# Optimization experiments

Measured on AMD Instinct MI355X. Metric: run time of the kernel, lower is better.

The kernel has to match this reference:

```python
import jax, jax.numpy as jnp
import numpy as np

B, N, S = 8, 512, 96
SD = TD = H = 256
NH, HD = 8, 32  # num_heads, head_dim
OUT = 4


def setup_inputs() -> dict:
    key = jax.random.key(0)
    ks = jax.random.split(key, 20)
    g = lambda k, shape: (jax.random.normal(k, shape, dtype=jnp.float32) * 0.02)
    return {
        "spatial_features": jax.random.normal(ks[0], (B, N, SD), dtype=jnp.float32),
        "temporal_features": jax.random.normal(ks[1], (B, S, TD), dtype=jnp.float32),
        "Ws": g(ks[2], (H, SD)),   "bs": g(ks[3], (H,)),
        "Wt": g(ks[4], (H, TD)),   "bt": g(ks[5], (H,)),
        "Win": g(ks[6], (3 * H, H)), "bin": g(ks[7], (3 * H,)),
        "Wao": g(ks[8], (H, H)),   "bao": g(ks[9], (H,)),
        "W1": g(ks[10], (H, H)),   "b1": g(ks[11], (H,)),
        "Wo1": g(ks[12], (H // 2, H)), "bo1": g(ks[13], (H // 2,)),
        "Wo2": g(ks[14], (OUT, H // 2)), "bo2": g(ks[15], (OUT,)),
    }


def reference(spatial_features, temporal_features, Ws, bs, Wt, bt, Win, bin, Wao, bao,
              W1, b1, Wo1, bo1, Wo2, bo2):
    # Projections
    sp = spatial_features @ Ws.T + bs          # [B, N, H]
    tp = temporal_features @ Wt.T + bt         # [B, S, H]
    # MultiheadAttention in_proj (batched over all N node-queries at once;
    # mathematically identical to the original per-node loop)
    Wq, Wk, Wv = Win[:H], Win[H:2 * H], Win[2 * H:]
    bq, bk, bv = bin[:H], bin[H:2 * H], bin[2 * H:]
    q = (sp @ Wq.T + bq).reshape(B, N, NH, HD)   # [B, N, h, d]
    k = (tp @ Wk.T + bk).reshape(B, S, NH, HD)   # [B, S, h, d]
    v = (tp @ Wv.T + bv).reshape(B, S, NH, HD)
    scale = 1.0 / np.sqrt(HD).astype(np.float32)
    logits = jnp.einsum('bnhd,bshd->bhns', q * scale, k)   # [B, h, N, S]
    attn = jax.nn.softmax(logits, axis=-1)
    ctx = jnp.einsum('bhns,bshd->bnhd', attn, v).reshape(B, N, H)
    attended = ctx @ Wao.T + bao               # [B, N, H] (out_proj)
    # fusion_layer: Linear + ReLU (dropout=identity in eval)
    fused = jax.nn.relu(attended @ W1.T + b1)  # [B, N, H]
    # output_layer: Linear -> ReLU -> Linear
    h2 = jax.nn.relu(fused @ Wo1.T + bo1)      # [B, N, H/2]
    y = h2 @ Wo2.T + bo2                       # [B, N, OUT]
    # original expands over seq_len BEFORE fusion_layer; since all layers are
    # pointwise over the (S, N) grid, compute once per node and broadcast.
    return jnp.broadcast_to(y[:, None, :, :], (B, S, N, OUT))
```

## Files before the change

kernel.cpp:

```cpp
#include <hip/hip_runtime.h>

#define BB 8
#define NN 512
#define SS 96
#define HH 256
#define NHD 8
#define HDD 32
#define OUTD 4

#define WSB_OFF  0
#define WTB_OFF  65536
#define WINB_OFF 131072
#define WAOB_OFF 327680
#define W1B_OFF  393216
#define WO1B_OFF 458752
#define BF_TOTAL 491520
#define QB_OFF   491520
#define KB_OFF   (QB_OFF + 1048576)
#define VTB_OFF  (KB_OFF + 196608)

typedef __attribute__((ext_vector_type(8))) short bf16x8;
typedef __attribute__((ext_vector_type(4))) float f32x4;

__device__ __forceinline__ unsigned short f2bf(float f) {
    unsigned int u = __float_as_uint(f);
    u = (u + 0x7FFFu + ((u >> 16) & 1u)) >> 16;
    return (unsigned short)u;
}

__global__ __launch_bounds__(256) void k_cast(
    const float* __restrict__ Ws, const float* __restrict__ Wt,
    const float* __restrict__ Win, const float* __restrict__ Wao,
    const float* __restrict__ W1, const float* __restrict__ Wo1,
    unsigned short* __restrict__ dst)
{
    int idx = blockIdx.x * 256 + threadIdx.x;
    for (int j4 = idx; j4 < BF_TOTAL / 4; j4 += 120 * 256) {
        int e = j4 * 4;
        const float* src; int off;
        if (e < 65536)       { src = Ws;  off = e; }
        else if (e < 131072) { src = Wt;  off = e - 65536; }
        else if (e < 327680) { src = Win; off = e - 131072; }
        else if (e < 393216) { src = Wao; off = e - 327680; }
        else if (e < 458752) { src = W1;  off = e - 393216; }
        else                 { src = Wo1; off = e - 458752; }
        float4 v = *(const float4*)(src + off);
        ushort4 o;
        o.x = f2bf(v.x); o.y = f2bf(v.y); o.z = f2bf(v.z); o.w = f2bf(v.w);
        *(ushort4*)(dst + e) = o;
    }
}

template<int NCT>
__device__ __forceinline__ void mfma_stage(
    const unsigned short* __restrict__ Asw,
    const unsigned short* __restrict__ Wb,
    int lane, int wave, f32x4 acc[NCT])
{
    const int row = lane & 15, kq = lane >> 4;
    #pragma unroll
    for (int ct = 0; ct < NCT; ++ct) acc[ct] = (f32x4){0.f, 0.f, 0.f, 0.f};
    #pragma unroll 2
    for (int kt = 0; kt < 8; ++kt) {
        const int slot = kt * 4 + kq;
        bf16x8 a = *(const bf16x8*)(Asw + row * 256 + ((slot ^ (row & 7)) << 3));
        #pragma unroll
        for (int ct = 0; ct < NCT; ++ct) {
            const unsigned short* wp =
                Wb + (size_t)((wave * NCT + ct) * 16 + row) * 256 + kt * 32 + kq * 8;
            bf16x8 b = *(const bf16x8*)wp;
            acc[ct] = __builtin_amdgcn_mfma_f32_16x16x32_bf16(a, b, acc[ct], 0, 0, 0);
        }
    }
}

template<int NCT, bool RELU>
__device__ __forceinline__ void epi_lds(
    unsigned short* __restrict__ OutSw, const float* __restrict__ bias,
    int lane, int wave, const f32x4 acc[NCT])
{
    const int col0 = lane & 15, rq = lane >> 4;
    #pragma unroll
    for (int ct = 0; ct < NCT; ++ct) {
        const int C = wave * NCT * 16 + ct * 16 + col0;
        const float bb = bias[C];
        const int slot = C >> 3, within = C & 7;
        #pragma unroll
        for (int r = 0; r < 4; ++r) {
            const int R = rq * 4 + r;
            float v = acc[ct][r] + bb;
            if (RELU) v = fmaxf(v, 0.f);
            OutSw[R * 256 + ((slot ^ (R & 7)) << 3) + within] = f2bf(v);
        }
    }
}

template<int NCT>
__device__ __forceinline__ void epi_gbf16(
    unsigned short* __restrict__ Og, const float* __restrict__ bias,
    int lane, int wave, const f32x4 acc[NCT])
{
    const int col0 = lane & 15, rq = lane >> 4;
    #pragma unroll
    for (int ct = 0; ct < NCT; ++ct) {
        const int C = wave * NCT * 16 + ct * 16 + col0;
        const float bb = bias[C];
        #pragma unroll
        for (int r = 0; r < 4; ++r) {
            const int R = rq * 4 + r;
            Og[(size_t)R * 256 + C] = f2bf(acc[ct][r] + bb);
        }
    }
}

__device__ __forceinline__ void stage_A(
    const float* __restrict__ Ag, unsigned short* __restrict__ Asw, int tid)
{
    #pragma unroll
    for (int ii = 0; ii < 4; ++ii) {
        int i = tid + ii * 256;
        int row = i >> 6, c4 = i & 63;
        float4 v = ((const float4*)(Ag + (size_t)row * 256))[c4];
        int col = c4 * 4;
        int slot = col >> 3, half = (col >> 2) & 1;
        ushort4 o;
        o.x = f2bf(v.x); o.y = f2bf(v.y); o.z = f2bf(v.z); o.w = f2bf(v.w);
        *(ushort4*)(Asw + row * 256 + ((slot ^ (row & 7)) << 3) + half * 4) = o;
    }
}

__global__ __launch_bounds__(256) void k_qkv(
    const float* __restrict__ spatial, const float* __restrict__ temporal,
    const float* __restrict__ bs, const float* __restrict__ bt,
    const float* __restrict__ bin,
    const unsigned short* __restrict__ bfw,
    unsigned short* __restrict__ qb, unsigned short* __restrict__ kb,
    unsigned short* __restrict__ vtb)
{
    __shared__ __align__(16) unsigned short A0[16 * 256];
    __shared__ __align__(16) unsigned short MID[16 * 256];
    const int tid = threadIdx.x, lane = tid & 63, wave = tid >> 6;
    f32x4 acc[4];

    if (blockIdx.x < 256) {
        const int r0 = blockIdx.x * 16;
        stage_A(spatial + (size_t)r0 * 256, A0, tid);
        __syncthreads();
        mfma_stage<4>(A0, bfw + WSB_OFF, lane, wave, acc);
        epi_lds<4, false>(MID, bs, lane, wave, acc);
        __syncthreads();
        mfma_stage<4>(MID, bfw + WINB_OFF, lane, wave, acc);
        epi_gbf16<4>(qb + (size_t)r0 * 256, bin, lane, wave, acc);
    } else {
        const int r0 = (blockIdx.x - 256) * 16;
        stage_A(temporal + (size_t)r0 * 256, A0, tid);
        __syncthreads();
        mfma_stage<4>(A0, bfw + WTB_OFF, lane, wave, acc);
        epi_lds<4, false>(MID, bt, lane, wave, acc);
        __syncthreads();
        mfma_stage<4>(MID, bfw + WINB_OFF + 65536, lane, wave, acc);
        epi_gbf16<4>(kb + (size_t)r0 * 256, bin + 256, lane, wave, acc);
        mfma_stage<4>(MID, bfw + WINB_OFF + 131072, lane, wave, acc);
        {
            const int bb_ = r0 / 96, s0 = r0 % 96;
            const int col0 = lane & 15, rq = lane >> 4;
            #pragma unroll
            for (int ct = 0; ct < 4; ++ct) {
                const int C = wave * 64 + ct * 16 + col0;
                const float bv = bin[512 + C];
                #pragma unroll
                for (int r = 0; r < 4; ++r) {
                    const int R = rq * 4 + r;
                    vtb[((size_t)(bb_ * 256 + C)) * 96 + s0 + R] = f2bf(acc[ct][r] + bv);
                }
            }
        }
    }
}

__global__ __launch_bounds__(256) void k_attnhead(
    const unsigned short* __restrict__ qb, const unsigned short* __restrict__ kb,
    const unsigned short* __restrict__ vtb, const unsigned short* __restrict__ bfw,
    const float* __restrict__ bao, const float* __restrict__ b1,
    const float* __restrict__ bo1,
    const float* __restrict__ Wo2, const float* __restrict__ bo2,
    float* __restrict__ out)
{
    __shared__ __align__(16) unsigned short A0[16 * 256];
    __shared__ __align__(16) unsigned short MID[16 * 256];
    __shared__ __align__(16) float H2[16 * 128];
    __shared__ __align__(16) unsigned short P[4][16 * 104];
    __shared__ __align__(16) float y[16][OUTD];
    const int tid = threadIdx.x, lane = tid & 63, wave = tid >> 6;
    const int b = blockIdx.x >> 5;
    const int n0 = (blockIdx.x & 31) * 16;
    const int cl = lane & 15, kq = lane >> 4;
    const float scale = 0.17677669529663687f;

    unsigned short* Pw = &P[wave][0];
    #pragma unroll
    for (int hh = 0; hh < 2; ++hh) {
        const int h = wave * 2 + hh;
        bf16x8 aq = *(const bf16x8*)(qb + (size_t)(b * NN + n0 + cl) * 256 + h * 32 + kq * 8);
        f32x4 l[6];
        #pragma unroll
        for (int t = 0; t < 6; ++t) {
            bf16x8 bk = *(const bf16x8*)(kb + (size_t)(b * SS + t * 16 + cl) * 256 + h * 32 + kq * 8);
            l[t] = __builtin_amdgcn_mfma_f32_16x16x32_bf16(aq, bk, (f32x4){0.f,0.f,0.f,0.f}, 0, 0, 0);
        }
        float pr[6][4];
        float sum[4] = {0.f, 0.f, 0.f, 0.f};
        #pragma unroll
        for (int t = 0; t < 6; ++t)
            #pragma unroll
            for (int r = 0; r < 4; ++r) {
                float p = __expf(l[t][r] * scale);
                pr[t][r] = p; sum[r] += p;
            }
        #pragma unroll
        for (int r = 0; r < 4; ++r) {
            float s = sum[r];
            s += __shfl_xor(s, 1); s += __shfl_xor(s, 2);
            s += __shfl_xor(s, 4); s += __shfl_xor(s, 8);
            sum[r] = 1.0f / s;
        }
        #pragma unroll
        for (int t = 0; t < 6; ++t)
            #pragma unroll
            for (int r = 0; r < 4; ++r)
                Pw[(kq * 4 + r) * 104 + t * 16 + cl] = f2bf(pr[t][r] * sum[r]);
        f32x4 c0 = (f32x4){0.f,0.f,0.f,0.f}, c1 = (f32x4){0.f,0.f,0.f,0.f};
        #pragma unroll
        for (int ks = 0; ks < 3; ++ks) {
            bf16x8 pa = *(const bf16x8*)(Pw + cl * 104 + ks * 32 + kq * 8);
            bf16x8 v0 = *(const bf16x8*)(vtb + (size_t)(b * 256 + h * 32 + cl) * 96 + ks * 32 + kq * 8);
            bf16x8 v1 = *(const bf16x8*)(vtb + (size_t)(b * 256 + h * 32 + 16 + cl) * 96 + ks * 32 + kq * 8);
            c0 = __builtin_amdgcn_mfma_f32_16x16x32_bf16(pa, v0, c0, 0, 0, 0);
            c1 = __builtin_amdgcn_mfma_f32_16x16x32_bf16(pa, v1, c1, 0, 0, 0);
        }
        #pragma unroll
        for (int dt = 0; dt < 2; ++dt) {
            const f32x4 cc = dt ? c1 : c0;
            const int C = h * 32 + dt * 16 + cl;
            const int slot = C >> 3, within = C & 7;
            #pragma unroll
            for (int r = 0; r < 4; ++r) {
                const int R = kq * 4 + r;
                A0[R * 256 + ((slot ^ (R & 7)) << 3) + within] = f2bf(cc[r]);
            }
        }
    }
    __syncthreads();

    f32x4 acc[4];
    mfma_stage<4>(A0, bfw + WAOB_OFF, lane, wave, acc);
    epi_lds<4, false>(MID, bao, lane, wave, acc);
    __syncthreads();
    mfma_stage<4>(MID, bfw + W1B_OFF, lane, wave, acc);
    epi_lds<4, true>(A0, b1, lane, wave, acc);
    __syncthreads();
    {
        f32x4 a2[2];
        mfma_stage<2>(A0, bfw + WO1B_OFF, lane, wave, a2);
        const int rq = lane >> 4;
        #pragma unroll
        for (int ct = 0; ct < 2; ++ct) {
            const int C = wave * 32 + ct * 16 + cl;
            const float bb = bo1[C];
            #pragma unroll
            for (int r = 0; r < 4; ++r) {
                const int R = rq * 4 + r;
                H2[R * 128 + C] = fmaxf(a2[ct][r] + bb, 0.f);
            }
        }
    }
    __syncthreads();
    if (tid < 64) {
        int r = tid >> 2, o = tid & 3;
        float a = 0.f;
        const float4* w4 = (const float4*)(Wo2 + (size_t)o * 128);
        const float4* h4 = (const float4*)(H2 + r * 128);
        for (int kk = 0; kk < 32; ++kk) {
            float4 w = w4[kk], hv = h4[kk];
            a += hv.x * w.x + hv.y * w.y + hv.z * w.z + hv.w * w.w;
        }
        y[r][o] = a + bo2[o];
    }
    __syncthreads();
    const int nbase = n0;
    for (int i = tid; i < 16 * SS; i += 256) {
        int s = i >> 4;
        int r = i & 15;
        *(float4*)(out + ((size_t)(b * SS + s) * NN + (nbase + r)) * OUTD) = *(const float4*)y[r];
    }
}

extern "C" void kernel_launch(void* const* d_in, const int* in_sizes, int n_in,
                              void* d_out, int out_size, void* d_ws, size_t ws_size,
                              hipStream_t stream) {
    const float* spatial  = (const float*)d_in[0];
    const float* temporal = (const float*)d_in[1];
    const float* Ws  = (const float*)d_in[2];
    const float* bs  = (const float*)d_in[3];
    const float* Wt  = (const float*)d_in[4];
    const float* bt  = (const float*)d_in[5];
    const float* Win = (const float*)d_in[6];
    const float* bin = (const float*)d_in[7];
    const float* Wao = (const float*)d_in[8];
    const float* bao = (const float*)d_in[9];
    const float* W1  = (const float*)d_in[10];
    const float* b1  = (const float*)d_in[11];
    const float* Wo1 = (const float*)d_in[12];
    const float* bo1 = (const float*)d_in[13];
    const float* Wo2 = (const float*)d_in[14];
    const float* bo2 = (const float*)d_in[15];
    float* out = (float*)d_out;
    unsigned short* wsu = (unsigned short*)d_ws;

    unsigned short* bfw = wsu;
    unsigned short* qb  = wsu + QB_OFF;
    unsigned short* kb  = wsu + KB_OFF;
    unsigned short* vtb = wsu + VTB_OFF;

    hipLaunchKernelGGL(k_cast, dim3(120), dim3(256), 0, stream,
                       Ws, Wt, Win, Wao, W1, Wo1, bfw);
    hipLaunchKernelGGL(k_qkv, dim3(304), dim3(256), 0, stream,
                       spatial, temporal, bs, bt, bin, bfw, qb, kb, vtb);
    hipLaunchKernelGGL(k_attnhead, dim3(256), dim3(256), 0, stream,
                       qb, kb, vtb, bfw, bao, b1, bo1, Wo2, bo2, out);
}
```

Baseline: 127.1 us.

## Fuse Q projection into attention kernel and merge weight cast with K/V prep

Moves the spatial projection and Q in-projection into the attention/head kernel, so Q stays in shared memory instead of going through global memory. The K/V projection now reads fp32 weights directly and casts them on the fly. It runs concurrently with the weight cast of the remaining matrices inside one kernel, which cuts three launches down to two. In exchange, each attention block does extra GEMM work before attention, and the K/V blocks redundantly convert weights per load.

```diff
diff --git a/kernel.cpp b/kernel.cpp
--- a/kernel.cpp
+++ b/kernel.cpp
@@ -9,15 +9,13 @@
 #define OUTD 4
 
 #define WSB_OFF  0
-#define WTB_OFF  65536
-#define WINB_OFF 131072
-#define WAOB_OFF 327680
-#define W1B_OFF  393216
-#define WO1B_OFF 458752
-#define BF_TOTAL 491520
-#define QB_OFF   491520
-#define KB_OFF   (QB_OFF + 1048576)
-#define VTB_OFF  (KB_OFF + 196608)
+#define WQB_OFF  65536
+#define WAOB_OFF 131072
+#define W1B_OFF  196608
+#define WO1B_OFF 262144
+#define CAST_TOTAL 294912
+#define KB_OFF   294912
+#define VTB_OFF  491520
 
 typedef __attribute__((ext_vector_type(8))) short bf16x8;
 typedef __attribute__((ext_vector_type(4))) float f32x4;
@@ -28,27 +26,14 @@
     return (unsigned short)u;
 }
 
-__global__ __launch_bounds__(256) void k_cast(
-    const float* __restrict__ Ws, const float* __restrict__ Wt,
-    const float* __restrict__ Win, const float* __restrict__ Wao,
-    const float* __restrict__ W1, const float* __restrict__ Wo1,
-    unsigned short* __restrict__ dst)
-{
-    int idx = blockIdx.x * 256 + threadIdx.x;
-    for (int j4 = idx; j4 < BF_TOTAL / 4; j4 += 120 * 256) {
-        int e = j4 * 4;
-        const float* src; int off;
-        if (e < 65536)       { src = Ws;  off = e; }
-        else if (e < 131072) { src = Wt;  off = e - 65536; }
-        else if (e < 327680) { src = Win; off = e - 131072; }
-        else if (e < 393216) { src = Wao; off = e - 327680; }
-        else if (e < 458752) { src = W1;  off = e - 393216; }
-        else                 { src = Wo1; off = e - 458752; }
-        float4 v = *(const float4*)(src + off);
-        ushort4 o;
-        o.x = f2bf(v.x); o.y = f2bf(v.y); o.z = f2bf(v.z); o.w = f2bf(v.w);
-        *(ushort4*)(dst + e) = o;
-    }
+__device__ __forceinline__ bf16x8 ldw8(const float* __restrict__ p) {
+    float4 a = *(const float4*)p, b = *(const float4*)(p + 4);
+    bf16x8 r;
+    r[0] = (short)f2bf(a.x); r[1] = (short)f2bf(a.y);
+    r[2] = (short)f2bf(a.z); r[3] = (short)f2bf(a.w);
+    r[4] = (short)f2bf(b.x); r[5] = (short)f2bf(b.y);
+    r[6] = (short)f2bf(b.z); r[7] = (short)f2bf(b.w);
+    return r;
 }
 
 template<int NCT>
@@ -69,6 +54,29 @@
             const unsigned short* wp =
                 Wb + (size_t)((wave * NCT + ct) * 16 + row) * 256 + kt * 32 + kq * 8;
             bf16x8 b = *(const bf16x8*)wp;
+            acc[ct] = __builtin_amdgcn_mfma_f32_16x16x32_bf16(a, b, acc[ct], 0, 0, 0);
+        }
+    }
+}
+
+template<int NCT>
+__device__ __forceinline__ void mfma_stage_f32w(
+    const unsigned short* __restrict__ Asw,
+    const float* __restrict__ Wf,
+    int lane, int wave, f32x4 acc[NCT])
+{
+    const int row = lane & 15, kq = lane >> 4;
+    #pragma unroll
+    for (int ct = 0; ct < NCT; ++ct) acc[ct] = (f32x4){0.f, 0.f, 0.f, 0.f};
+    #pragma unroll 2
+    for (int kt = 0; kt < 8; ++kt) {
+        const int slot = kt * 4 + kq;
+        bf16x8 a = *(const bf16x8*)(Asw + row * 256 + ((slot ^ (row & 7)) << 3));
+        #pragma unroll
+        for (int ct = 0; ct < NCT; ++ct) {
+            const float* wp =
+                Wf + (size_t)((wave * NCT + ct) * 16 + row) * 256 + kt * 32 + kq * 8;
+            bf16x8 b = ldw8(wp);
             acc[ct] = __builtin_amdgcn_mfma_f32_16x16x32_bf16(a, b, acc[ct], 0, 0, 0);
         }
     }
@@ -129,38 +137,30 @@
     }
 }
 
-__global__ __launch_bounds__(256) void k_qkv(
-    const float* __restrict__ spatial, const float* __restrict__ temporal,
-    const float* __restrict__ bs, const float* __restrict__ bt,
-    const float* __restrict__ bin,
-    const unsigned short* __restrict__ bfw,
-    unsigned short* __restrict__ qb, unsigned short* __restrict__ kb,
-    unsigned short* __restrict__ vtb)
-{
-    __shared__ __align__(16) unsigned short A0[16 * 256];
-    __shared__ __align__(16) unsigned short MID[16 * 256];
-    const int tid = threadIdx.x, lane = tid & 63, wave = tid >> 6;
-    f32x4 acc[4];
-
-    if (blockIdx.x < 256) {
+__global__ __launch_bounds__(256) void k_prep(
+    const float* __restrict__ temporal,
+    const float* __restrict__ bt, const float* __restrict__ bin,
+    const float* __restrict__ Wt, const float* __restrict__ Win,
+    const float* __restrict__ Ws, const float* __restrict__ Wao,
+    const float* __restrict__ W1, const float* __restrict__ Wo1,
+    unsigned short* __restrict__ kb, unsigned short* __restrict__ vtb,
+    unsigned short* __restrict__ bfw)
+{
+    const int tid = threadIdx.x;
+    if (blockIdx.x < 48) {
+        __shared__ __align__(16) unsigned short A0[16 * 256];
+        __shared__ __align__(16) unsigned short MID[16 * 256];
+        const int lane = tid & 63, wave = tid >> 6;
         const int r0 = blockIdx.x * 16;
-        stage_A(spatial + (size_t)r0 * 256, A0, tid);
-        __syncthreads();
-        mfma_stage<4>(A0, bfw + WSB_OFF, lane, wave, acc);
-        epi_lds<4, false>(MID, bs, lane, wave, acc);
-        __syncthreads();
-        mfma_stage<4>(MID, bfw + WINB_OFF, lane, wave, acc);
-        epi_gbf16<4>(qb + (size_t)r0 * 256, bin, lane, wave, acc);
-    } else {
-        const int r0 = (blockIdx.x - 256) * 16;
+        f32x4 acc[4];
         stage_A(temporal + (size_t)r0 * 256, A0, tid);
         __syncthreads();
-        mfma_stage<4>(A0, bfw + WTB_OFF, lane, wave, acc);
+        mfma_stage_f32w<4>(A0, Wt, lane, wave, acc);
         epi_lds<4, false>(MID, bt, lane, wave, acc);
         __syncthreads();
-        mfma_stage<4>(MID, bfw + WINB_OFF + 65536, lane, wave, acc);
+        mfma_stage_f32w<4>(MID, Win + 65536, lane, wave, acc);
         epi_gbf16<4>(kb + (size_t)r0 * 256, bin + 256, lane, wave, acc);
-        mfma_stage<4>(MID, bfw + WINB_OFF + 131072, lane, wave, acc);
+        mfma_stage_f32w<4>(MID, Win + 131072, lane, wave, acc);
         {
             const int bb_ = r0 / 96, s0 = r0 % 96;
             const int col0 = lane & 15, rq = lane >> 4;
@@ -175,12 +175,29 @@
                 }
             }
         }
-    }
-}
-
-__global__ __launch_bounds__(256) void k_attnhead(
-    const unsigned short* __restrict__ qb, const unsigned short* __restrict__ kb,
-    const unsigned short* __restrict__ vtb, const unsigned short* __restrict__ bfw,
+    } else {
+        int idx = (blockIdx.x - 48) * 256 + tid;
+        for (int j4 = idx; j4 < CAST_TOTAL / 4; j4 += 48 * 256) {
+            int e = j4 * 4;
+            const float* src; int off;
+            if (e < 65536)       { src = Ws;  off = e; }
+            else if (e < 131072) { src = Win; off = e - 65536; }
+            else if (e < 196608) { src = Wao; off = e - 131072; }
+            else if (e < 262144) { src = W1;  off = e - 196608; }
+            else                 { src = Wo1; off = e - 262144; }
+            float4 v = *(const float4*)(src + off);
+            ushort4 o;
+            o.x = f2bf(v.x); o.y = f2bf(v.y); o.z = f2bf(v.z); o.w = f2bf(v.w);
+            *(ushort4*)(bfw + e) = o;
+        }
+    }
+}
+
+__global__ __launch_bounds__(256) void k_main(
+    const float* __restrict__ spatial,
+    const float* __restrict__ bs, const float* __restrict__ bin,
+    const unsigned short* __restrict__ bfw,
+    const unsigned short* __restrict__ kb, const unsigned short* __restrict__ vtb,
     const float* __restrict__ bao, const float* __restrict__ b1,
     const float* __restrict__ bo1,
     const float* __restrict__ Wo2, const float* __restrict__ bo2,
@@ -188,20 +205,31 @@
 {
     __shared__ __align__(16) unsigned short A0[16 * 256];
     __shared__ __align__(16) unsigned short MID[16 * 256];
+    __shared__ __align__(16) unsigned short Q[16 * 256];
+    __shared__ __align__(16) unsigned short P[4][16 * 104];
     __shared__ __align__(16) float H2[16 * 128];
-    __shared__ __align__(16) unsigned short P[4][16 * 104];
     __shared__ __align__(16) float y[16][OUTD];
     const int tid = threadIdx.x, lane = tid & 63, wave = tid >> 6;
     const int b = blockIdx.x >> 5;
     const int n0 = (blockIdx.x & 31) * 16;
     const int cl = lane & 15, kq = lane >> 4;
     const float scale = 0.17677669529663687f;
+    f32x4 acc[4];
+
+    stage_A(spatial + (size_t)(b * NN + n0) * 256, A0, tid);
+    __syncthreads();
+    mfma_stage<4>(A0, bfw + WSB_OFF, lane, wave, acc);
+    epi_lds<4, false>(MID, bs, lane, wave, acc);
+    __syncthreads();
+    mfma_stage<4>(MID, bfw + WQB_OFF, lane, wave, acc);
+    epi_lds<4, false>(Q, bin, lane, wave, acc);
 
     unsigned short* Pw = &P[wave][0];
     #pragma unroll
     for (int hh = 0; hh < 2; ++hh) {
         const int h = wave * 2 + hh;
-        bf16x8 aq = *(const bf16x8*)(qb + (size_t)(b * NN + n0 + cl) * 256 + h * 32 + kq * 8);
+        const int slotq = h * 4 + kq;
+        bf16x8 aq = *(const bf16x8*)(Q + cl * 256 + ((slotq ^ (cl & 7)) << 3));
         f32x4 l[6];
         #pragma unroll
         for (int t = 0; t < 6; ++t) {
@@ -252,7 +280,6 @@
     }
     __syncthreads();
 
-    f32x4 acc[4];
     mfma_stage<4>(A0, bfw + WAOB_OFF, lane, wave, acc);
     epi_lds<4, false>(MID, bao, lane, wave, acc);
     __syncthreads();
@@ -287,11 +314,10 @@
         y[r][o] = a + bo2[o];
     }
     __syncthreads();
-    const int nbase = n0;
     for (int i = tid; i < 16 * SS; i += 256) {
         int s = i >> 4;
         int r = i & 15;
-        *(float4*)(out + ((size_t)(b * SS + s) * NN + (nbase + r)) * OUTD) = *(const float4*)y[r];
+        *(float4*)(out + ((size_t)(b * SS + s) * NN + (n0 + r)) * OUTD) = *(const float4*)y[r];
     }
 }
 
@@ -318,14 +344,13 @@
     unsigned short* wsu = (unsigned short*)d_ws;
 
     unsigned short* bfw = wsu;
-    unsigned short* qb  = wsu + QB_OFF;
     unsigned short* kb  = wsu + KB_OFF;
     unsigned short* vtb = wsu + VTB_OFF;
 
-    hipLaunchKernelGGL(k_cast, dim3(120), dim3(256), 0, stream,
-                       Ws, Wt, Win, Wao, W1, Wo1, bfw);
-    hipLaunchKernelGGL(k_qkv, dim3(304), dim3(256), 0, stream,
-                       spatial, temporal, bs, bt, bin, bfw, qb, kb, vtb);
-    hipLaunchKernelGGL(k_attnhead, dim3(256), dim3(256), 0, stream,
-                       qb, kb, vtb, bfw, bao, b1, bo1, Wo2, bo2, out);
-}
+    hipLaunchKernelGGL(k_prep, dim3(96), dim3(256), 0, stream,
+                       temporal, bt, bin, Wt, Win, Ws, Wao, W1, Wo1,
+                       kb, vtb, bfw);
+    hipLaunchKernelGGL(k_main, dim3(256), dim3(256), 0, stream,
+                       spatial, bs, bin, bfw, kb, vtb,
+                       bao, b1, bo1, Wo2, bo2, out);
+}
```

Result: slower. 146.4 us (+15.1%).

## Pre-multiply consecutive linear weights to fold projection chains into single GEMMs

Applied to the files above, without the earlier changes.

Folds the consecutive linear layers algebraically: Wq·Ws, Wk·Wt, Wv·Wt and W1·Wao are multiplied once per call in a new weight-fusion kernel, which also folds the matching biases. This halves the per-row GEMM chains in the QKV and post-attention stages. Blocks widen to 512 threads (8 waves, one head per wave), and K and V are split across separate blocks for more parallelism. The fused weight product is done in fp32 on the GPU on every call, which adds a small dense matmul, and rounding to bf16 now happens on the product rather than on each factor.

```diff
diff --git a/kernel.cpp b/kernel.cpp
--- a/kernel.cpp
+++ b/kernel.cpp
@@ -8,16 +8,15 @@
 #define HDD 32
 #define OUTD 4
 
-#define WSB_OFF  0
-#define WTB_OFF  65536
-#define WINB_OFF 131072
-#define WAOB_OFF 327680
-#define W1B_OFF  393216
-#define WO1B_OFF 458752
-#define BF_TOTAL 491520
-#define QB_OFF   491520
-#define KB_OFF   (QB_OFF + 1048576)
+#define WQS_OFF  0
+#define WKT_OFF  65536
+#define WVT_OFF  131072
+#define W1AO_OFF 196608
+#define WO1B_OFF 262144
+#define FB_OFF   294912
+#define KB_OFF   296960
 #define VTB_OFF  (KB_OFF + 196608)
+#define QB_OFF   (VTB_OFF + 196608)
 
 typedef __attribute__((ext_vector_type(8))) short bf16x8;
 typedef __attribute__((ext_vector_type(4))) float f32x4;
@@ -26,29 +25,6 @@
     unsigned int u = __float_as_uint(f);
     u = (u + 0x7FFFu + ((u >> 16) & 1u)) >> 16;
     return (unsigned short)u;
-}
-
-__global__ __launch_bounds__(256) void k_cast(
-    const float* __restrict__ Ws, const float* __restrict__ Wt,
-    const float* __restrict__ Win, const float* __restrict__ Wao,
-    const float* __restrict__ W1, const float* __restrict__ Wo1,
-    unsigned short* __restrict__ dst)
-{
-    int idx = blockIdx.x * 256 + threadIdx.x;
-    for (int j4 = idx; j4 < BF_TOTAL / 4; j4 += 120 * 256) {
-        int e = j4 * 4;
-        const float* src; int off;
-        if (e < 65536)       { src = Ws;  off = e; }
-        else if (e < 131072) { src = Wt;  off = e - 65536; }
-        else if (e < 327680) { src = Win; off = e - 131072; }
-        else if (e < 393216) { src = Wao; off = e - 327680; }
-        else if (e < 458752) { src = W1;  off = e - 393216; }
-        else                 { src = Wo1; off = e - 458752; }
-        float4 v = *(const float4*)(src + off);
-        ushort4 o;
-        o.x = f2bf(v.x); o.y = f2bf(v.y); o.z = f2bf(v.z); o.w = f2bf(v.w);
-        *(ushort4*)(dst + e) = o;
-    }
 }
 
 template<int NCT>
@@ -113,12 +89,13 @@
     }
 }
 
+template<int NT>
 __device__ __forceinline__ void stage_A(
     const float* __restrict__ Ag, unsigned short* __restrict__ Asw, int tid)
 {
     #pragma unroll
-    for (int ii = 0; ii < 4; ++ii) {
-        int i = tid + ii * 256;
+    for (int ii = 0; ii < 1024 / NT; ++ii) {
+        int i = tid + ii * NT;
         int row = i >> 6, c4 = i & 63;
         float4 v = ((const float4*)(Ag + (size_t)row * 256))[c4];
         int col = c4 * 4;
@@ -129,78 +106,131 @@
     }
 }
 
-__global__ __launch_bounds__(256) void k_qkv(
+__global__ __launch_bounds__(512) void k_wfuse(
+    const float* __restrict__ Ws, const float* __restrict__ bs,
+    const float* __restrict__ Wt, const float* __restrict__ bt,
+    const float* __restrict__ Win, const float* __restrict__ bin,
+    const float* __restrict__ Wao, const float* __restrict__ bao,
+    const float* __restrict__ W1, const float* __restrict__ b1,
+    const float* __restrict__ Wo1,
+    unsigned short* __restrict__ bfw, float* __restrict__ fb)
+{
+    const int tid = threadIdx.x;
+    if (blockIdx.x < 128) {
+        const int m = blockIdx.x >> 5, t = blockIdx.x & 31;
+        const int i = t * 8 + (tid >> 6);
+        const int j = tid & 63;
+        const float* A = (m == 0) ? Win : (m == 1) ? (Win + 65536)
+                       : (m == 2) ? (Win + 131072) : W1;
+        const float* B = (m == 0) ? Ws : (m == 3) ? Wao : Wt;
+        float a0 = 0.f, a1 = 0.f, a2 = 0.f, a3 = 0.f;
+        const float* Ar = A + (size_t)i * 256;
+        #pragma unroll 4
+        for (int k = 0; k < 256; ++k) {
+            float av = Ar[k];
+            const float* Br = B + (size_t)k * 256 + j;
+            a0 += av * Br[0];
+            a1 += av * Br[64];
+            a2 += av * Br[128];
+            a3 += av * Br[192];
+        }
+        unsigned short* dst = bfw + m * 65536 + (size_t)i * 256 + j;
+        dst[0]   = f2bf(a0);
+        dst[64]  = f2bf(a1);
+        dst[128] = f2bf(a2);
+        dst[192] = f2bf(a3);
+    } else if (blockIdx.x < 136) {
+        int idx = (blockIdx.x - 128) * 512 + tid;
+        for (int e4 = idx; e4 < 8192; e4 += 8 * 512) {
+            int e = e4 * 4;
+            float4 v = *(const float4*)(Wo1 + e);
+            ushort4 o;
+            o.x = f2bf(v.x); o.y = f2bf(v.y); o.z = f2bf(v.z); o.w = f2bf(v.w);
+            *(ushort4*)(bfw + WO1B_OFF + e) = o;
+        }
+    } else {
+        const int wave = tid >> 6, lane = tid & 63;
+        const int g = (blockIdx.x - 136) * 8 + wave;
+        const int m = g >> 8, j = g & 255;
+        const float* Wrow; const float* vec; float add;
+        if (m == 0)      { Wrow = Win + (size_t)j * 256;          vec = bs;  add = bin[j]; }
+        else if (m == 1) { Wrow = Win + (size_t)(256 + j) * 256;  vec = bt;  add = bin[256 + j]; }
+        else if (m == 2) { Wrow = Win + (size_t)(512 + j) * 256;  vec = bt;  add = bin[512 + j]; }
+        else             { Wrow = W1 + (size_t)j * 256;           vec = bao; add = b1[j]; }
+        float s = 0.f;
+        #pragma unroll
+        for (int q = 0; q < 4; ++q) s += Wrow[q * 64 + lane] * vec[q * 64 + lane];
+        s += __shfl_xor(s, 1);  s += __shfl_xor(s, 2);  s += __shfl_xor(s, 4);
+        s += __shfl_xor(s, 8);  s += __shfl_xor(s, 16); s += __shfl_xor(s, 32);
+        if (lane == 0) fb[m * 256 + j] = s + add;
+    }
+}
+
+__global__ __launch_bounds__(512) void k_qkv(
     const float* __restrict__ spatial, const float* __restrict__ temporal,
-    const float* __restrict__ bs, const float* __restrict__ bt,
-    const float* __restrict__ bin,
-    const unsigned short* __restrict__ bfw,
+    const unsigned short* __restrict__ bfw, const float* __restrict__ fb,
     unsigned short* __restrict__ qb, unsigned short* __restrict__ kb,
     unsigned short* __restrict__ vtb)
 {
     __shared__ __align__(16) unsigned short A0[16 * 256];
-    __shared__ __align__(16) unsigned short MID[16 * 256];
     const int tid = threadIdx.x, lane = tid & 63, wave = tid >> 6;
-    f32x4 acc[4];
+    f32x4 acc[2];
 
     if (blockIdx.x < 256) {
         const int r0 = blockIdx.x * 16;
-        stage_A(spatial + (size_t)r0 * 256, A0, tid);
+        stage_A<512>(spatial + (size_t)r0 * 256, A0, tid);
         __syncthreads();
-        mfma_stage<4>(A0, bfw + WSB_OFF, lane, wave, acc);
-        epi_lds<4, false>(MID, bs, lane, wave, acc);
+        mfma_stage<2>(A0, bfw + WQS_OFF, lane, wave, acc);
+        epi_gbf16<2>(qb + (size_t)r0 * 256, fb, lane, wave, acc);
+    } else {
+        const int blk = blockIdx.x - 256;
+        const int m = blk >> 1, which = blk & 1;
+        const int r0 = m * 16;
+        stage_A<512>(temporal + (size_t)r0 * 256, A0, tid);
         __syncthreads();
-        mfma_stage<4>(MID, bfw + WINB_OFF, lane, wave, acc);
-        epi_gbf16<4>(qb + (size_t)r0 * 256, bin, lane, wave, acc);
-    } else {
-        const int r0 = (blockIdx.x - 256) * 16;
-        stage_A(temporal + (size_t)r0 * 256, A0, tid);
-        __syncthreads();
-        mfma_stage<4>(A0, bfw + WTB_OFF, lane, wave, acc);
-        epi_lds<4, false>(MID, bt, lane, wave, acc);
-        __syncthreads();
-        mfma_stage<4>(MID, bfw + WINB_OFF + 65536, lane, wave, acc);
-        epi_gbf16<4>(kb + (size_t)r0 * 256, bin + 256, lane, wave, acc);
-        mfma_stage<4>(MID, bfw + WINB_OFF + 131072, lane, wave, acc);
-        {
+        if (which == 0) {
+            mfma_stage<2>(A0, bfw + WKT_OFF, lane, wave, acc);
+            epi_gbf16<2>(kb + (size_t)r0 * 256, fb + 256, lane, wave, acc);
+        } else {
+            mfma_stage<2>(A0, bfw + WVT_OFF, lane, wave, acc);
             const int bb_ = r0 / 96, s0 = r0 % 96;
-            const int col0 = lane & 15, rq = lane >> 4;
+            const int cl = lane & 15, rq = lane >> 4;
             #pragma unroll
-            for (int ct = 0; ct < 4; ++ct) {
-                const int C = wave * 64 + ct * 16 + col0;
-                const float bv = bin[512 + C];
+            for (int ct = 0; ct < 2; ++ct) {
+                const int Cl = wave * 32 + ct * 16 + cl;
+                const float bv = fb[512 + Cl];
                 #pragma unroll
                 for (int r = 0; r < 4; ++r) {
                     const int R = rq * 4 + r;
-                    vtb[((size_t)(bb_ * 256 + C)) * 96 + s0 + R] = f2bf(acc[ct][r] + bv);
+                    vtb[((size_t)(bb_ * 256 + Cl)) * 96 + s0 + R] = f2bf(acc[ct][r] + bv);
                 }
             }
         }
     }
 }
 
-__global__ __launch_bounds__(256) void k_attnhead(
+__global__ __launch_bounds__(512) void k_attnmlp(
     const unsigned short* __restrict__ qb, const unsigned short* __restrict__ kb,
     const unsigned short* __restrict__ vtb, const unsigned short* __restrict__ bfw,
-    const float* __restrict__ bao, const float* __restrict__ b1,
-    const float* __restrict__ bo1,
-    const float* __restrict__ Wo2, const float* __restrict__ bo2,
-    float* __restrict__ out)
+    const float* __restrict__ fb,
+    const float* __restrict__ bo1, const float* __restrict__ Wo2,
+    const float* __restrict__ bo2, float* __restrict__ out)
 {
     __shared__ __align__(16) unsigned short A0[16 * 256];
     __shared__ __align__(16) unsigned short MID[16 * 256];
+    __shared__ __align__(16) unsigned short P[8][16 * 104];
     __shared__ __align__(16) float H2[16 * 128];
-    __shared__ __align__(16) unsigned short P[4][16 * 104];
     __shared__ __align__(16) float y[16][OUTD];
     const int tid = threadIdx.x, lane = tid & 63, wave = tid >> 6;
     const int b = blockIdx.x >> 5;
     const int n0 = (blockIdx.x & 31) * 16;
     const int cl = lane & 15, kq = lane >> 4;
     const float scale = 0.17677669529663687f;
+    f32x4 acc[2];
 
     unsigned short* Pw = &P[wave][0];
-    #pragma unroll
-    for (int hh = 0; hh < 2; ++hh) {
-        const int h = wave * 2 + hh;
+    {
+        const int h = wave;
         bf16x8 aq = *(const bf16x8*)(qb + (size_t)(b * NN + n0 + cl) * 256 + h * 32 + kq * 8);
         f32x4 l[6];
         #pragma unroll
@@ -252,26 +282,19 @@
     }
     __syncthreads();
 
-    f32x4 acc[4];
-    mfma_stage<4>(A0, bfw + WAOB_OFF, lane, wave, acc);
-    epi_lds<4, false>(MID, bao, lane, wave, acc);
-    __syncthreads();
-    mfma_stage<4>(MID, bfw + W1B_OFF, lane, wave, acc);
-    epi_lds<4, true>(A0, b1, lane, wave, acc);
+    mfma_stage<2>(A0, bfw + W1AO_OFF, lane, wave, acc);
+    epi_lds<2, true>(MID, fb + 768, lane, wave, acc);
     __syncthreads();
     {
-        f32x4 a2[2];
-        mfma_stage<2>(A0, bfw + WO1B_OFF, lane, wave, a2);
+        f32x4 a1[1];
+        mfma_stage<1>(MID, bfw + WO1B_OFF, lane, wave, a1);
         const int rq = lane >> 4;
-        #pragma unroll
-        for (int ct = 0; ct < 2; ++ct) {
-            const int C = wave * 32 + ct * 16 + cl;
-            const float bb = bo1[C];
-            #pragma unroll
-            for (int r = 0; r < 4; ++r) {
-                const int R = rq * 4 + r;
-                H2[R * 128 + C] = fmaxf(a2[ct][r] + bb, 0.f);
-            }
+        const int C = wave * 16 + cl;
+        const float bb = bo1[C];
+        #pragma unroll
+        for (int r = 0; r < 4; ++r) {
+            const int R = rq * 4 + r;
+            H2[R * 128 + C] = fmaxf(a1[0][r] + bb, 0.f);
         }
     }
     __syncthreads();
@@ -287,11 +310,10 @@
         y[r][o] = a + bo2[o];
     }
     __syncthreads();
-    const int nbase = n0;
-    for (int i = tid; i < 16 * SS; i += 256) {
+    for (int i = tid; i < 16 * SS; i += 512) {
         int s = i >> 4;
         int r = i & 15;
-        *(float4*)(out + ((size_t)(b * SS + s) * NN + (nbase + r)) * OUTD) = *(const float4*)y[r];
+        *(float4*)(out + ((size_t)(b * SS + s) * NN + (n0 + r)) * OUTD) = *(const float4*)y[r];
     }
 }
 
@@ -318,14 +340,16 @@
     unsigned short* wsu = (unsigned short*)d_ws;
 
     unsigned short* bfw = wsu;
-    unsigned short* qb  = wsu + QB_OFF;
+    float* fb = (float*)(wsu + FB_OFF);
     unsigned short* kb  = wsu + KB_OFF;
     unsigned short* vtb = wsu + VTB_OFF;
-
-    hipLaunchKernelGGL(k_cast, dim3(120), dim3(256), 0, stream,
-                       Ws, Wt, Win, Wao, W1, Wo1, bfw);
-    hipLaunchKernelGGL(k_qkv, dim3(304), dim3(256), 0, stream,
-                       spatial, temporal, bs, bt, bin, bfw, qb, kb, vtb);
-    hipLaunchKernelGGL(k_attnhead, dim3(256), dim3(256), 0, stream,
-                       qb, kb, vtb, bfw, bao, b1, bo1, Wo2, bo2, out);
-}
+    unsigned short* qb  = wsu + QB_OFF;
+
+    hipLaunchKernelGGL(k_wfuse, dim3(264), dim3(512), 0, stream,
+                       Ws, bs, Wt, bt, Win, bin, Wao, bao, W1, b1, Wo1,
+                       bfw, fb);
+    hipLaunchKernelGGL(k_qkv, dim3(352), dim3(512), 0, stream,
+                       spatial, temporal, bfw, fb, qb, kb, vtb);
+    hipLaunchKernelGGL(k_attnmlp, dim3(256), dim3(512), 0, stream,
+                       qb, kb, vtb, bfw, fb, bo1, Wo2, bo2, out);
+}
```

Measured after the change: 128.4 us. No clear change (+1.0%).
